# Performance work log

Hardware: AMD Instinct MI355X
Metric: run time of the kernel (lower is better)

Reference implementation:

```python
import jax, jax.numpy as jnp
import numpy as np

K = 16          # neighbors per node
EPS = 1e-5      # BatchNorm eps
BN_SCALE = 1.0 / np.sqrt(1.0 + EPS)  # eval BN with running mean=0, var=1


def _knn_idx(x, k):
    # x: [B, N, d] -> idx [B, N, k] of k nearest neighbors (self excluded)
    sq = jnp.sum(x * x, axis=-1)                               # [B, N]
    d2 = sq[:, :, None] + sq[:, None, :] - 2.0 * jnp.einsum('bnd,bmd->bnm', x, x)
    n = x.shape[1]
    d2 = jnp.where(jnp.eye(n, dtype=bool)[None], jnp.inf, d2)  # no self loops
    _, idx = jax.lax.top_k(-d2, k)
    return idx


def _edge_conv(x, idx, W, b, g, be):
    # PyG EdgeConv: max_j MLP([x_i, x_j - x_i]); MLP = Linear+BN(eval)+ReLU
    xj = jax.vmap(lambda xb, ib: xb[ib])(x, idx)               # [B, N, k, d]
    xi = x[:, :, None, :]
    m = jnp.concatenate([jnp.broadcast_to(xi, xj.shape), xj - xi], axis=-1)
    h = m @ W + b                                              # [B, N, k, out]
    h = g * (h * BN_SCALE) + be                                # eval BatchNorm
    h = jax.nn.relu(h)
    return jnp.max(h, axis=2)                                  # scatter-max over k


def setup_inputs() -> dict:
    key = jax.random.key(0)
    ks = jax.random.split(key, 16)
    B, N, D, C = 128, 256, 6, 12

    def w(k_, shape, fan_in):
        return (jax.random.normal(k_, shape, jnp.float32) / np.sqrt(fan_in)).astype(jnp.float32)

    inp = {
        'x':   jax.random.normal(ks[0], (B, N, D), jnp.float32),
        'W1':  w(ks[1], (2 * 6, 64), 12),   'b1': jnp.zeros((64,), jnp.float32),
        'g1':  jnp.ones((64,), jnp.float32), 'be1': jnp.zeros((64,), jnp.float32),
        'W2':  w(ks[2], (2 * 64, 128), 128), 'b2': jnp.zeros((128,), jnp.float32),
        'g2':  jnp.ones((128,), jnp.float32), 'be2': jnp.zeros((128,), jnp.float32),
        'W3':  w(ks[3], (2 * 128, 256), 256), 'b3': jnp.zeros((256,), jnp.float32),
        'g3':  jnp.ones((256,), jnp.float32), 'be3': jnp.zeros((256,), jnp.float32),
        'Wf1': w(ks[4], (256, 128), 256),    'bf1': jnp.zeros((128,), jnp.float32),
        'gf':  jnp.ones((128,), jnp.float32), 'bef': jnp.zeros((128,), jnp.float32),
        'Wf2': w(ks[5], (128, C), 128),      'bf2': jnp.zeros((C,), jnp.float32),
    }
    return inp


def reference(x, W1, b1, g1, be1, W2, b2, g2, be2, W3, b3, g3, be3,
              Wf1, bf1, gf, bef, Wf2, bf2):
    h = _edge_conv(x, _knn_idx(x, K), W1, b1, g1, be1)   # [B, N, 64]
    h = _edge_conv(h, _knn_idx(h, K), W2, b2, g2, be2)   # [B, N, 128]
    h = _edge_conv(h, _knn_idx(h, K), W3, b3, g3, be3)   # [B, N, 256]
    p = jnp.max(h, axis=1)                               # global_max_pool [B, 256]
    f = jax.nn.relu(gf * ((p @ Wf1 + bf1) * BN_SCALE) + bef)
    return f @ Wf2 + bf2                                 # [B, num_classes]
```

## Files before the change

### kernel.cpp

```cpp
#include <hip/hip_runtime.h>
#include <cstdint>
#include <cstddef>

#define KNN 16
#define NPTS 256
#define NBATCH 128

static constexpr float BN_SCALE_F = 0.9999950000374997f;

__device__ inline unsigned int f32_ord(float f) {
    unsigned int u = __float_as_uint(f);
    return (u & 0x80000000u) ? ~u : (u | 0x80000000u);
}

__device__ __forceinline__ int wmap(int n) { return n + 4 * (n >> 4); }

template<int D>
__global__ __launch_bounds__(256) void sq_kernel(const float* __restrict__ x,
                                                 float* __restrict__ sq) {
    const int t = blockIdx.x * 256 + threadIdx.x;
    const float* r = x + (size_t)t * D;
    float s = 0.f;
    #pragma unroll
    for (int d = 0; d < D; ++d) s = fmaf(r[d], r[d], s);
    sq[t] = s;
}

template<int D>
__global__ __launch_bounds__(256) void knn_fused_kernel(
        const float* __restrict__ x, const float* __restrict__ sq,
        int* __restrict__ idx) {
    constexpr int KS = (D >= 16) ? 16 : D;
    constexpr int NSTEP = D / KS;
    const int t  = threadIdx.x;
    const int tx = t & 15, ty = t >> 4;
    const int sr = t >> 2, sc = t & 3;
    const int b  = blockIdx.x >> 2;
    const int i0 = (blockIdx.x & 3) * 64;
    const int base = b * NPTS;

    __shared__ float As[D][68];
    __shared__ float Bs[KS][68];
    __shared__ float d2L[64][65];
    __shared__ unsigned char Mi[64][68];

    if constexpr (D % 16 == 0) {
        #pragma unroll
        for (int q = 0; q < D / 16; ++q) {
            const int e = t + q * 256;
            const int r = e / (D / 4);
            const int cq = (e % (D / 4)) * 4;
            const float4 v = *(const float4*)(x + (size_t)(base + i0 + r) * D + cq);
            As[cq + 0][r] = v.x; As[cq + 1][r] = v.y;
            As[cq + 2][r] = v.z; As[cq + 3][r] = v.w;
        }
    } else {
        for (int e = t; e < 64 * D; e += 256) {
            const int r = e / D, c = e % D;
            As[c][r] = x[(size_t)(base + i0 + r) * D + c];
        }
    }

    const int br = t >> 2, bcq = (t & 3) * 4;
    float4 pb4;
    float  pbs[2];
    if constexpr (D % 16 == 0) {
        pb4 = *(const float4*)(x + (size_t)(base + br) * D + bcq);
    } else {
        #pragma unroll
        for (int u = 0; u < 2; ++u) {
            const int e = t + u * 256;
            if (e < 64 * KS) {
                const int r = e / KS, c = e % KS;
                pbs[u] = x[(size_t)(base + r) * D + c];
            }
        }
    }

    float sqi[4];
    #pragma unroll
    for (int m = 0; m < 4; ++m) sqi[m] = sq[base + i0 + ty * 4 + m];

    unsigned int Lv[16], Li[16];
    #pragma unroll
    for (int q = 0; q < 16; ++q) { Lv[q] = 0xFFFFFFFFu; Li[q] = 0u; }

    for (int jt = 0; jt < 4; ++jt) {
        const int j0 = jt * 64;
        float acc[4][4] = {};
        for (int s = 0; s < NSTEP; ++s) {
            if constexpr (D % 16 == 0) {
                Bs[bcq + 0][br] = pb4.x; Bs[bcq + 1][br] = pb4.y;
                Bs[bcq + 2][br] = pb4.z; Bs[bcq + 3][br] = pb4.w;
            } else {
                #pragma unroll
                for (int u = 0; u < 2; ++u) {
                    const int e = t + u * 256;
                    if (e < 64 * KS) {
                        const int r = e / KS, c = e % KS;
                        Bs[c][r] = pbs[u];
                    }
                }
            }
            __syncthreads();

            int njt = jt, ns = s + 1;
            if (ns == NSTEP) { ns = 0; njt = jt + 1; }
            if (njt < 4) {
                if constexpr (D % 16 == 0) {
                    pb4 = *(const float4*)(x + (size_t)(base + njt * 64 + br) * D
                                           + ns * KS + bcq);
                } else {
                    #pragma unroll
                    for (int u = 0; u < 2; ++u) {
                        const int e = t + u * 256;
                        if (e < 64 * KS) {
                            const int r = e / KS, c = e % KS;
                            pbs[u] = x[(size_t)(base + njt * 64 + r) * D + c];
                        }
                    }
                }
            }

            #pragma unroll
            for (int kk = 0; kk < KS; ++kk) {
                const float4 av = *(const float4*)&As[s * KS + kk][ty * 4];
                const float4 bv = *(const float4*)&Bs[kk][tx * 4];
                const float am[4] = {av.x, av.y, av.z, av.w};
                const float bm[4] = {bv.x, bv.y, bv.z, bv.w};
                #pragma unroll
                for (int m = 0; m < 4; ++m)
                    #pragma unroll
                    for (int n = 0; n < 4; ++n)
                        acc[m][n] = fmaf(am[m], bm[n], acc[m][n]);
            }
            __syncthreads();
        }

        float sqj[4];
        #pragma unroll
        for (int n = 0; n < 4; ++n) sqj[n] = sq[base + j0 + tx * 4 + n];
        #pragma unroll
        for (int m = 0; m < 4; ++m) {
            const int gi = i0 + ty * 4 + m;
            #pragma unroll
            for (int n = 0; n < 4; ++n) {
                float v = (sqi[m] + sqj[n]) - 2.f * acc[m][n];
                if (gi == j0 + tx * 4 + n) v = INFINITY;
                d2L[ty * 4 + m][tx * 4 + n] = v;
            }
        }
        __syncthreads();

        #pragma unroll
        for (int i = 0; i < 16; ++i) {
            const unsigned int v = f32_ord(d2L[sr][sc * 16 + i]);
            const unsigned int j = (unsigned int)(j0 + sc * 16 + i);
            #pragma unroll
            for (int q = 15; q >= 1; --q) {
                const bool a = v < Lv[q];
                const bool c = v < Lv[q - 1];
                Lv[q] = a ? (c ? Lv[q - 1] : v) : Lv[q];
                Li[q] = a ? (c ? Li[q - 1] : j) : Li[q];
            }
            const bool a0 = v < Lv[0];
            Lv[0] = a0 ? v : Lv[0];
            Li[0] = a0 ? j : Li[0];
        }
    }

    __syncthreads();
    #pragma unroll
    for (int q = 0; q < 16; ++q) {
        d2L[sr][sc * 16 + q] = __uint_as_float(Lv[q]);
        Mi[sr][sc * 16 + q]  = (unsigned char)Li[q];
    }
    __syncthreads();

    if (t < 64) {
        const int row = t;
        int h[4];
        unsigned int cv[4], ci[4];
        #pragma unroll
        for (int c = 0; c < 4; ++c) {
            h[c]  = 0;
            cv[c] = __float_as_uint(d2L[row][c * 16]);
            ci[c] = Mi[row][c * 16];
        }
        int outj[16];
        #pragma unroll
        for (int rd = 0; rd < 16; ++rd) {
            unsigned int bv = cv[0], bi = ci[0];
            int bc = 0;
            #pragma unroll
            for (int c = 1; c < 4; ++c) {
                const bool tk = (cv[c] < bv) | ((cv[c] == bv) & (ci[c] < bi));
                bv = tk ? cv[c] : bv;
                bi = tk ? ci[c] : bi;
                bc = tk ? c     : bc;
            }
            outj[rd] = (int)bi;
            #pragma unroll
            for (int c = 0; c < 4; ++c) {
                if (c == bc) {
                    const int hn = h[c] + 1;
                    h[c] = hn;
                    if (hn < 16) {
                        cv[c] = __float_as_uint(d2L[row][c * 16 + hn]);
                        ci[c] = Mi[row][c * 16 + hn];
                    } else {
                        cv[c] = 0xFFFFFFFFu;
                    }
                }
            }
        }
        int4* op = (int4*)(idx + (size_t)(base + i0 + row) * KNN);
        op[0] = make_int4(outj[0],  outj[1],  outj[2],  outj[3]);
        op[1] = make_int4(outj[4],  outj[5],  outj[6],  outj[7]);
        op[2] = make_int4(outj[8],  outj[9],  outj[10], outj[11]);
        op[3] = make_int4(outj[12], outj[13], outj[14], outj[15]);
    }
}

template<int D, int C>
__global__ __launch_bounds__(256) void mlp_gemm_kernel(
        const float* __restrict__ x, const float* __restrict__ W,
        const float* __restrict__ bias, const float* __restrict__ g,
        const float* __restrict__ be,
        float* __restrict__ A, float* __restrict__ Bv) {
    constexpr int BM = 128;
    constexpr int KT = (D >= 16) ? 16 : D;
    const int t  = threadIdx.x;
    const int m0 = blockIdx.x * BM;
    const int n0 = blockIdx.y * 128;
    const int tx = t & 15;
    const int ty = t >> 4;

    __shared__ float Xs[KT][BM + 4];
    __shared__ float Ws[KT][160];

    float acc[8][8] = {};

    for (int k0 = 0; k0 < D; k0 += KT) {
        if constexpr (D % 16 == 0) {
            const int r  = t >> 1;
            const int cq = (t & 1) * 8;
            const float* src = x + (size_t)(m0 + r) * D + k0 + cq;
            const float4 v0 = *(const float4*)(src);
            const float4 v1 = *(const float4*)(src + 4);
            Xs[cq + 0][r] = v0.x; Xs[cq + 1][r] = v0.y;
            Xs[cq + 2][r] = v0.z; Xs[cq + 3][r] = v0.w;
            Xs[cq + 4][r] = v1.x; Xs[cq + 5][r] = v1.y;
            Xs[cq + 6][r] = v1.z; Xs[cq + 7][r] = v1.w;
        } else {
            for (int e = t; e < BM * KT; e += 256) {
                const int r = e / KT, c = e % KT;
                Xs[c][r] = x[(size_t)(m0 + r) * D + k0 + c];
            }
        }
        if constexpr (D % 16 == 0) {
            const int wk = t >> 4;
            const int nq = (t & 15) * 8;
            const int mb = wmap(nq);
            const int gn = n0 + nq;
            const int kr = k0 + wk;
            if (gn < C) {
                const float* pt = W + (size_t)kr * C + gn;
                const float* pb = W + (size_t)(D + kr) * C + gn;
                const float4 t0 = *(const float4*)(pt);
                const float4 t1 = *(const float4*)(pt + 4);
                const float4 b0 = *(const float4*)(pb);
                const float4 b1 = *(const float4*)(pb + 4);
                *(float4*)&Ws[wk][mb]     = make_float4(t0.x - b0.x, t0.y - b0.y,
                                                        t0.z - b0.z, t0.w - b0.w);
                *(float4*)&Ws[wk][mb + 4] = make_float4(t1.x - b1.x, t1.y - b1.y,
                                                        t1.z - b1.z, t1.w - b1.w);
            } else {
                const float* pb = W + (size_t)(D + kr) * C + (gn - C);
                *(float4*)&Ws[wk][mb]     = *(const float4*)(pb);
                *(float4*)&Ws[wk][mb + 4] = *(const float4*)(pb + 4);
            }
        } else {
            for (int e = t; e < KT * 128; e += 256) {
                const int k = e >> 7, n = e & 127;
                const int gn = n0 + n, kr = k0 + k;
                Ws[k][wmap(n)] = (gn < C)
                    ? W[(size_t)kr * C + gn] - W[(size_t)(D + kr) * C + gn]
                    : W[(size_t)(D + kr) * C + (gn - C)];
            }
        }
        __syncthreads();

        const int mc = wmap(tx * 8);
        #pragma unroll
        for (int kk = 0; kk < KT; ++kk) {
            float xm[8], wn[8];
            *(float4*)&xm[0] = *(const float4*)&Xs[kk][ty * 8];
            *(float4*)&xm[4] = *(const float4*)&Xs[kk][ty * 8 + 4];
            *(float4*)&wn[0] = *(const float4*)&Ws[kk][mc];
            *(float4*)&wn[4] = *(const float4*)&Ws[kk][mc + 4];
            #pragma unroll
            for (int m = 0; m < 8; ++m)
                #pragma unroll
                for (int n = 0; n < 8; ++n)
                    acc[m][n] = fmaf(xm[m], wn[n], acc[m][n]);
        }
        __syncthreads();
    }

    const int gn = n0 + tx * 8;
    if (gn < C) {
        float fac[8];
        #pragma unroll
        for (int e = 0; e < 8; ++e) fac[e] = g[gn + e] * BN_SCALE_F;
        #pragma unroll
        for (int m = 0; m < 8; ++m) {
            float o[8];
            #pragma unroll
            for (int e = 0; e < 8; ++e) o[e] = fac[e] * acc[m][e];
            float* dst = A + (size_t)(m0 + ty * 8 + m) * C + gn;
            *(float4*)(dst)     = make_float4(o[0], o[1], o[2], o[3]);
            *(float4*)(dst + 4) = make_float4(o[4], o[5], o[6], o[7]);
        }
    } else {
        const int cb = gn - C;
        float fac[8], bb[8], bee[8];
        #pragma unroll
        for (int e = 0; e < 8; ++e) {
            fac[e] = g[cb + e] * BN_SCALE_F;
            bb[e]  = bias[cb + e];
            bee[e] = be[cb + e];
        }
        #pragma unroll
        for (int m = 0; m < 8; ++m) {
            float o[8];
            #pragma unroll
            for (int e = 0; e < 8; ++e)
                o[e] = fmaf(fac[e], acc[m][e] + bb[e], bee[e]);
            float* dst = Bv + (size_t)(m0 + ty * 8 + m) * C + cb;
            *(float4*)(dst)     = make_float4(o[0], o[1], o[2], o[3]);
            *(float4*)(dst + 4) = make_float4(o[4], o[5], o[6], o[7]);
        }
    }
}

template<int C>
__global__ __launch_bounds__(C) void combine_kernel(
        const float* A, const float* __restrict__ Bv,
        const int* __restrict__ idx, float* out) {
    const int bi = blockIdx.x;
    const int c  = threadIdx.x;
    __shared__ int nbr[KNN];
    if (c < KNN) nbr[c] = idx[(size_t)bi * KNN + c];
    __syncthreads();
    const int b0 = bi & ~255;
    float mx = -INFINITY;
    #pragma unroll
    for (int kk = 0; kk < KNN; ++kk)
        mx = fmaxf(mx, Bv[(size_t)(b0 + nbr[kk]) * C + c]);
    float a = A[(size_t)bi * C + c];
    out[(size_t)bi * C + c] = fmaxf(a + mx, 0.f);
}

__global__ __launch_bounds__(256) void head_kernel(
        const float* __restrict__ h3, const float* __restrict__ Wf1,
        const float* __restrict__ bf1, const float* __restrict__ gf,
        const float* __restrict__ bef, const float* __restrict__ Wf2,
        const float* __restrict__ bf2, float* __restrict__ out) {
    const int b   = blockIdx.x;
    const int tid = threadIdx.x;
    __shared__ float p[256];
    __shared__ float f[128];
    const float* hb = h3 + (size_t)b * NPTS * 256;
    float mx = -INFINITY;
    for (int n = 0; n < NPTS; ++n) mx = fmaxf(mx, hb[(size_t)n * 256 + tid]);
    p[tid] = mx;
    __syncthreads();
    if (tid < 128) {
        float acc = bf1[tid];
        for (int d = 0; d < 256; ++d)
            acc = fmaf(p[d], Wf1[(size_t)d * 128 + tid], acc);
        float v = gf[tid] * (acc * BN_SCALE_F) + bef[tid];
        f[tid] = fmaxf(v, 0.f);
    }
    __syncthreads();
    if (tid < 12) {
        float acc = bf2[tid];
        for (int d = 0; d < 128; ++d)
            acc = fmaf(f[d], Wf2[(size_t)d * 12 + tid], acc);
        out[(size_t)b * 12 + tid] = acc;
    }
}

extern "C" void kernel_launch(void* const* d_in, const int* in_sizes, int n_in,
                              void* d_out, int out_size, void* d_ws, size_t ws_size,
                              hipStream_t stream) {
    const float* x   = (const float*)d_in[0];
    const float* W1  = (const float*)d_in[1];
    const float* b1  = (const float*)d_in[2];
    const float* g1  = (const float*)d_in[3];
    const float* be1 = (const float*)d_in[4];
    const float* W2  = (const float*)d_in[5];
    const float* b2  = (const float*)d_in[6];
    const float* g2  = (const float*)d_in[7];
    const float* be2 = (const float*)d_in[8];
    const float* W3  = (const float*)d_in[9];
    const float* b3  = (const float*)d_in[10];
    const float* g3  = (const float*)d_in[11];
    const float* be3 = (const float*)d_in[12];
    const float* Wf1 = (const float*)d_in[13];
    const float* bf1 = (const float*)d_in[14];
    const float* gf  = (const float*)d_in[15];
    const float* bef = (const float*)d_in[16];
    const float* Wf2 = (const float*)d_in[17];
    const float* bf2 = (const float*)d_in[18];
    float* out = (float*)d_out;

    char* ws = (char*)d_ws;
    const size_t idx_bytes = (size_t)NBATCH * NPTS * KNN * sizeof(int);
    const size_t reg_bytes = (size_t)NBATCH * NPTS * 256 * sizeof(float);
    int*   idx = (int*)ws;
    float* R1  = (float*)(ws + idx_bytes);
    float* R2  = (float*)(ws + idx_bytes + reg_bytes);
    float* R3  = (float*)(ws + idx_bytes + 2 * reg_bytes);
    float* sqb = (float*)(ws + idx_bytes + 3 * reg_bytes);

    const int BN = NBATCH * NPTS;
    const int KNN_GRID = NBATCH * 4;
    const int MB = BN / 128;

    sq_kernel<6><<<BN / 256, 256, 0, stream>>>(x, sqb);
    knn_fused_kernel<6><<<KNN_GRID, 256, 0, stream>>>(x, sqb, idx);
    mlp_gemm_kernel<6, 64><<<dim3(MB, 1), 256, 0, stream>>>(
        x, W1, b1, g1, be1, R1, R2);
    combine_kernel<64><<<BN, 64, 0, stream>>>(R1, R2, idx, R1);

    sq_kernel<64><<<BN / 256, 256, 0, stream>>>(R1, sqb);
    knn_fused_kernel<64><<<KNN_GRID, 256, 0, stream>>>(R1, sqb, idx);
    mlp_gemm_kernel<64, 128><<<dim3(MB, 2), 256, 0, stream>>>(
        R1, W2, b2, g2, be2, R2, R3);
    combine_kernel<128><<<BN, 128, 0, stream>>>(R2, R3, idx, R2);

    sq_kernel<128><<<BN / 256, 256, 0, stream>>>(R2, sqb);
    knn_fused_kernel<128><<<KNN_GRID, 256, 0, stream>>>(R2, sqb, idx);
    mlp_gemm_kernel<128, 256><<<dim3(MB, 4), 256, 0, stream>>>(
        R2, W3, b3, g3, be3, R3, R1);
    combine_kernel<256><<<BN, 256, 0, stream>>>(R3, R1, idx, R3);

    head_kernel<<<NBATCH, 256, 0, stream>>>(R3, Wf1, bf1, gf, bef, Wf2, bf2, out);
}
```

Baseline: 478.6 us.

## Enlarge kNN tile to 128 rows with 8x8 register blocking and double-buffered LDS

```diff
diff --git a/kernel.cpp b/kernel.cpp
--- a/kernel.cpp
+++ b/kernel.cpp
@@ -32,130 +32,146 @@
         int* __restrict__ idx) {
     constexpr int KS = (D >= 16) ? 16 : D;
     constexpr int NSTEP = D / KS;
+    constexpr int NLOADG = (128 * KS + 255) / 256;
     const int t  = threadIdx.x;
     const int tx = t & 15, ty = t >> 4;
-    const int sr = t >> 2, sc = t & 3;
-    const int b  = blockIdx.x >> 2;
-    const int i0 = (blockIdx.x & 3) * 64;
+    const int sr = t >> 1, sc = t & 1;
+    const int b  = blockIdx.x >> 1;
+    const int i0 = (blockIdx.x & 1) * 128;
     const int base = b * NPTS;
 
-    __shared__ float As[D][68];
-    __shared__ float Bs[KS][68];
-    __shared__ float d2L[64][65];
-    __shared__ unsigned char Mi[64][68];
-
+    __shared__ float As[2][KS][132];
+    __shared__ float Bs[2][KS][132];
+    __shared__ float d2L[128][132];
+    __shared__ unsigned char Mi[128][36];
+
+    float4 pa[2], pb[2];
+    float  pas[NLOADG], pbs[NLOADG];
     if constexpr (D % 16 == 0) {
         #pragma unroll
-        for (int q = 0; q < D / 16; ++q) {
-            const int e = t + q * 256;
-            const int r = e / (D / 4);
-            const int cq = (e % (D / 4)) * 4;
-            const float4 v = *(const float4*)(x + (size_t)(base + i0 + r) * D + cq);
-            As[cq + 0][r] = v.x; As[cq + 1][r] = v.y;
-            As[cq + 2][r] = v.z; As[cq + 3][r] = v.w;
+        for (int u = 0; u < 2; ++u) {
+            const int e = t + u * 256, r = e >> 2, cq = (e & 3) * 4;
+            pa[u] = *(const float4*)(x + (size_t)(base + i0 + r) * D + cq);
+            pb[u] = *(const float4*)(x + (size_t)(base + r) * D + cq);
         }
     } else {
-        for (int e = t; e < 64 * D; e += 256) {
-            const int r = e / D, c = e % D;
-            As[c][r] = x[(size_t)(base + i0 + r) * D + c];
-        }
-    }
-
-    const int br = t >> 2, bcq = (t & 3) * 4;
-    float4 pb4;
-    float  pbs[2];
-    if constexpr (D % 16 == 0) {
-        pb4 = *(const float4*)(x + (size_t)(base + br) * D + bcq);
-    } else {
-        #pragma unroll
-        for (int u = 0; u < 2; ++u) {
+        #pragma unroll
+        for (int u = 0; u < NLOADG; ++u) {
             const int e = t + u * 256;
-            if (e < 64 * KS) {
+            if (e < 128 * KS) {
                 const int r = e / KS, c = e % KS;
+                pas[u] = x[(size_t)(base + i0 + r) * D + c];
                 pbs[u] = x[(size_t)(base + r) * D + c];
             }
         }
     }
 
-    float sqi[4];
+    float sqi[8];
     #pragma unroll
-    for (int m = 0; m < 4; ++m) sqi[m] = sq[base + i0 + ty * 4 + m];
+    for (int m = 0; m < 8; ++m) sqi[m] = sq[base + i0 + ty * 8 + m];
 
     unsigned int Lv[16], Li[16];
     #pragma unroll
     for (int q = 0; q < 16; ++q) { Lv[q] = 0xFFFFFFFFu; Li[q] = 0u; }
 
-    for (int jt = 0; jt < 4; ++jt) {
-        const int j0 = jt * 64;
-        float acc[4][4] = {};
+    for (int jt = 0; jt < 2; ++jt) {
+        const int j0 = jt * 128;
+        float acc[8][8] = {};
         for (int s = 0; s < NSTEP; ++s) {
+            const int g   = jt * NSTEP + s;
+            const int buf = g & 1;
             if constexpr (D % 16 == 0) {
-                Bs[bcq + 0][br] = pb4.x; Bs[bcq + 1][br] = pb4.y;
-                Bs[bcq + 2][br] = pb4.z; Bs[bcq + 3][br] = pb4.w;
+                #pragma unroll
+                for (int u = 0; u < 2; ++u) {
+                    const int e = t + u * 256, r = e >> 2, cq = (e & 3) * 4;
+                    As[buf][cq + 0][r] = pa[u].x; As[buf][cq + 1][r] = pa[u].y;
+                    As[buf][cq + 2][r] = pa[u].z; As[buf][cq + 3][r] = pa[u].w;
+                    Bs[buf][cq + 0][r] = pb[u].x; Bs[buf][cq + 1][r] = pb[u].y;
+                    Bs[buf][cq + 2][r] = pb[u].z; Bs[buf][cq + 3][r] = pb[u].w;
+                }
             } else {
                 #pragma unroll
-                for (int u = 0; u < 2; ++u) {
+                for (int u = 0; u < NLOADG; ++u) {
                     const int e = t + u * 256;
-                    if (e < 64 * KS) {
+                    if (e < 128 * KS) {
                         const int r = e / KS, c = e % KS;
-                        Bs[c][r] = pbs[u];
+                        As[buf][c][r] = pas[u];
+                        Bs[buf][c][r] = pbs[u];
                     }
                 }
             }
-            __syncthreads();
-
-            int njt = jt, ns = s + 1;
-            if (ns == NSTEP) { ns = 0; njt = jt + 1; }
-            if (njt < 4) {
-                if constexpr (D % 16 == 0) {
-                    pb4 = *(const float4*)(x + (size_t)(base + njt * 64 + br) * D
-                                           + ns * KS + bcq);
-                } else {
-                    #pragma unroll
-                    for (int u = 0; u < 2; ++u) {
-                        const int e = t + u * 256;
-                        if (e < 64 * KS) {
-                            const int r = e / KS, c = e % KS;
-                            pbs[u] = x[(size_t)(base + njt * 64 + r) * D + c];
+
+            {
+                const int gn2 = g + 1;
+                const int njt = gn2 / NSTEP, ns = gn2 % NSTEP;
+                if (njt < 2) {
+                    if constexpr (D % 16 == 0) {
+                        #pragma unroll
+                        for (int u = 0; u < 2; ++u) {
+                            const int e = t + u * 256, r = e >> 2, cq = (e & 3) * 4;
+                            pa[u] = *(const float4*)(x + (size_t)(base + i0 + r) * D
+                                                     + ns * KS + cq);
+                            pb[u] = *(const float4*)(x + (size_t)(base + njt * 128 + r) * D
+                                                     + ns * KS + cq);
+                        }
+                    } else {
+                        #pragma unroll
+                        for (int u = 0; u < NLOADG; ++u) {
+                            const int e = t + u * 256;
+                            if (e < 128 * KS) {
+                                const int r = e / KS, c = e % KS;
+                                pas[u] = x[(size_t)(base + i0 + r) * D + c];
+                                pbs[u] = x[(size_t)(base + njt * 128 + r) * D + c];
+                            }
                         }
                     }
                 }
             }
 
+            __syncthreads();
+
             #pragma unroll
             for (int kk = 0; kk < KS; ++kk) {
-                const float4 av = *(const float4*)&As[s * KS + kk][ty * 4];
-                const float4 bv = *(const float4*)&Bs[kk][tx * 4];
-                const float am[4] = {av.x, av.y, av.z, av.w};
-                const float bm[4] = {bv.x, bv.y, bv.z, bv.w};
+                float am[8], bm[8];
+                *(float4*)&am[0] = *(const float4*)&As[buf][kk][ty * 8];
+                *(float4*)&am[4] = *(const float4*)&As[buf][kk][ty * 8 + 4];
+                *(float4*)&bm[0] = *(const float4*)&Bs[buf][kk][tx * 4];
+                *(float4*)&bm[4] = *(const float4*)&Bs[buf][kk][64 + tx * 4];
                 #pragma unroll
-                for (int m = 0; m < 4; ++m)
+                for (int m = 0; m < 8; ++m)
                     #pragma unroll
-                    for (int n = 0; n < 4; ++n)
+                    for (int n = 0; n < 8; ++n)
                         acc[m][n] = fmaf(am[m], bm[n], acc[m][n]);
             }
-            __syncthreads();
-        }
-
-        float sqj[4];
-        #pragma unroll
-        for (int n = 0; n < 4; ++n) sqj[n] = sq[base + j0 + tx * 4 + n];
-        #pragma unroll
-        for (int m = 0; m < 4; ++m) {
-            const int gi = i0 + ty * 4 + m;
+        }
+
+        float sqj[8];
+        #pragma unroll
+        for (int n = 0; n < 4; ++n) {
+            sqj[n]     = sq[base + j0 + tx * 4 + n];
+            sqj[n + 4] = sq[base + j0 + 64 + tx * 4 + n];
+        }
+        #pragma unroll
+        for (int m = 0; m < 8; ++m) {
+            const int gi = i0 + ty * 8 + m;
+            float o0[4], o1[4];
             #pragma unroll
             for (int n = 0; n < 4; ++n) {
-                float v = (sqi[m] + sqj[n]) - 2.f * acc[m][n];
-                if (gi == j0 + tx * 4 + n) v = INFINITY;
-                d2L[ty * 4 + m][tx * 4 + n] = v;
-            }
+                float v0 = (sqi[m] + sqj[n])     - 2.f * acc[m][n];
+                float v1 = (sqi[m] + sqj[n + 4]) - 2.f * acc[m][n + 4];
+                if (gi == j0 + tx * 4 + n)      v0 = INFINITY;
+                if (gi == j0 + 64 + tx * 4 + n) v1 = INFINITY;
+                o0[n] = v0; o1[n] = v1;
+            }
+            *(float4*)&d2L[ty * 8 + m][tx * 4]      = make_float4(o0[0], o0[1], o0[2], o0[3]);
+            *(float4*)&d2L[ty * 8 + m][64 + tx * 4] = make_float4(o1[0], o1[1], o1[2], o1[3]);
         }
         __syncthreads();
 
-        #pragma unroll
-        for (int i = 0; i < 16; ++i) {
-            const unsigned int v = f32_ord(d2L[sr][sc * 16 + i]);
-            const unsigned int j = (unsigned int)(j0 + sc * 16 + i);
+        #pragma unroll 4
+        for (int i = 0; i < 64; ++i) {
+            const unsigned int v = f32_ord(d2L[sr][sc * 64 + i]);
+            const unsigned int j = (unsigned int)(j0 + sc * 64 + i);
             #pragma unroll
             for (int q = 15; q >= 1; --q) {
                 const bool a = v < Lv[q];
@@ -177,12 +193,12 @@
     }
     __syncthreads();
 
-    if (t < 64) {
+    if (t < 128) {
         const int row = t;
-        int h[4];
-        unsigned int cv[4], ci[4];
-        #pragma unroll
-        for (int c = 0; c < 4; ++c) {
+        int h[2];
+        unsigned int cv[2], ci[2];
+        #pragma unroll
+        for (int c = 0; c < 2; ++c) {
             h[c]  = 0;
             cv[c] = __float_as_uint(d2L[row][c * 16]);
             ci[c] = Mi[row][c * 16];
@@ -190,18 +206,11 @@
         int outj[16];
         #pragma unroll
         for (int rd = 0; rd < 16; ++rd) {
-            unsigned int bv = cv[0], bi = ci[0];
-            int bc = 0;
-            #pragma unroll
-            for (int c = 1; c < 4; ++c) {
-                const bool tk = (cv[c] < bv) | ((cv[c] == bv) & (ci[c] < bi));
-                bv = tk ? cv[c] : bv;
-                bi = tk ? ci[c] : bi;
-                bc = tk ? c     : bc;
-            }
-            outj[rd] = (int)bi;
-            #pragma unroll
-            for (int c = 0; c < 4; ++c) {
+            const bool tk = (cv[1] < cv[0]) | ((cv[1] == cv[0]) & (ci[1] < ci[0]));
+            const int bc = tk ? 1 : 0;
+            outj[rd] = (int)(tk ? ci[1] : ci[0]);
+            #pragma unroll
+            for (int c = 0; c < 2; ++c) {
                 if (c == bc) {
                     const int hn = h[c] + 1;
                     h[c] = hn;
@@ -426,7 +435,7 @@
     float* sqb = (float*)(ws + idx_bytes + 3 * reg_bytes);
 
     const int BN = NBATCH * NPTS;
-    const int KNN_GRID = NBATCH * 4;
+    const int KNN_GRID = NBATCH * 2;
     const int MB = BN / 128;
 
     sq_kernel<6><<<BN / 256, 256, 0, stream>>>(x, sqb);
```

Result: faster. 450.4 us (-5.9%).
